# Optimization experiments

Measured on AMD Instinct MI355X. Metric: run time of the kernel, lower is better.

The kernel has to match this reference:

```python
import jax, jax.numpy as jnp
import numpy as np

INF = 1e9
GAMMA, ALPHA, RADIUS = 2.0, 0.25, 1.5
STRIDES = (8, 16, 32, 64, 128)
IMG = 256
SIZES = ((-1.0, 64.0), (64.0, 128.0), (128.0, 256.0), (256.0, 512.0), (512.0, INF))


def _level_meta():
    # per-level 3D point grids, stride*radius per point, size-of-interest per point
    pts, spt, soi = [], [], []
    for s, (lo, hi) in zip(STRIDES, SIZES):
        n = IMG // s
        ax = (np.arange(n) + 0.5) * s
        zz, yy, xx = np.meshgrid(ax, ax, ax, indexing='ij')
        p = np.stack([xx.ravel(), yy.ravel(), zz.ravel()], 1)
        pts.append(p)
        spt.append(np.full(p.shape[0], s * RADIUS))
        soi.append(np.tile(np.array([lo, hi]), (p.shape[0], 1)))
    return (np.concatenate(pts).astype(np.float32),
            np.concatenate(spt).astype(np.float32),
            np.concatenate(soi).astype(np.float32))


def setup_inputs() -> dict:
    key = jax.random.key(0)
    ks = jax.random.split(key, 8)
    B, G, C = 4, 48, 8
    loc_np, spt_np, soi_np = _level_meta()
    N = loc_np.shape[0]  # 37448
    ctr = jax.random.uniform(ks[0], (B, G, 3), minval=32.0, maxval=224.0)
    half = jax.random.uniform(ks[1], (B, G, 3), minval=8.0, maxval=96.0)
    bboxes = jnp.concatenate([ctr - half, ctr + half], -1)  # valid xyzxyz boxes
    return {
        'locations': jnp.asarray(loc_np),
        'cls_pred': jax.random.normal(ks[2], (B, N, C), dtype=jnp.float32),
        'box_pred': jax.random.uniform(ks[3], (B, N, 6), minval=1.0, maxval=64.0),
        'center_pred': jax.random.normal(ks[4], (B, N), dtype=jnp.float32),
        'bboxes': bboxes,
        'gt_labels': jax.random.randint(ks[5], (B, G), 1, C + 1, dtype=jnp.int32),
        'gt_centers': ctr,
        'strides_pt': jnp.asarray(spt_np),
        'soi': jnp.asarray(soi_np),
    }


def _targets_one_image(loc, spt, soi, bb, lab):
    # loc [N,3], bb [G,6] -> label [N], box_target [N,6]
    xs, ys, zs = loc[:, 0], loc[:, 1], loc[:, 2]
    l = xs[:, None] - bb[None, :, 0]
    t = ys[:, None] - bb[None, :, 1]
    f = zs[:, None] - bb[None, :, 2]
    r = bb[None, :, 3] - xs[:, None]
    b = bb[None, :, 4] - ys[:, None]
    a = bb[None, :, 5] - zs[:, None]
    box_t = jnp.stack([l, t, f, r, b, a], 2)  # [N,G,6]
    # center sampling (get_sample_region): clip center box by gt box, test inside
    c = (bb[:, :3] + bb[:, 3:]) * 0.5  # [G,3]
    s = spt[:, None, None]  # [N,1,1] stride*radius per location
    cmin = jnp.maximum(c[None] - s, bb[None, :, :3])  # [N,G,3]
    cmax = jnp.minimum(c[None] + s, bb[None, :, 3:])
    d = jnp.concatenate([loc[:, None] - cmin, cmax - loc[:, None]], -1)  # [N,G,6]
    is_in = d.min(-1) > 0
    max_t = box_t.max(2)
    cared = (max_t >= soi[:, :1]) & (max_t <= soi[:, 1:2])
    area = jnp.prod(bb[:, 3:] - bb[:, :3], -1)  # [G]
    l2a = jnp.where(is_in & cared, area[None], INF)
    gt_id = jnp.argmin(l2a, 1)
    min_a = jnp.min(l2a, 1)
    box_target = jnp.take_along_axis(box_t, gt_id[:, None, None], 1)[:, 0]
    label = jnp.where(min_a == INF, 0, lab[gt_id])
    return label, box_target


def _focal_sum(logits, labels):
    # SigmoidFocalLoss, class ids 1..C, label 0 = background
    C = logits.shape[1]
    cr = jnp.arange(1, C + 1)
    pos = labels[:, None] == cr[None, :]
    p = jax.nn.sigmoid(logits)
    lp = jax.nn.log_sigmoid(logits)
    lnp = jax.nn.log_sigmoid(-logits)
    loss = jnp.where(pos, -ALPHA * (1.0 - p) ** GAMMA * lp,
                     -(1.0 - ALPHA) * p ** GAMMA * lnp)
    return loss.sum()


def _centerness(bt):
    lr = bt[:, jnp.array([0, 3])]
    tb = bt[:, jnp.array([1, 4])]
    fb = bt[:, jnp.array([2, 5])]
    c = (lr.min(1) / lr.max(1)) * (tb.min(1) / tb.max(1)) * (fb.min(1) / fb.max(1))
    return jnp.sqrt(jnp.clip(c, 1e-8, 1.0))


def _iou_loss(pred, tgt):
    # 3D IoU loss on (l,t,f,r,b,a) distances, -log(iou)
    pv = (pred[:, 0] + pred[:, 3]) * (pred[:, 1] + pred[:, 4]) * (pred[:, 2] + pred[:, 5])
    tv = (tgt[:, 0] + tgt[:, 3]) * (tgt[:, 1] + tgt[:, 4]) * (tgt[:, 2] + tgt[:, 5])
    m = jnp.minimum(pred, tgt)
    inter = (m[:, 0] + m[:, 3]) * (m[:, 1] + m[:, 4]) * (m[:, 2] + m[:, 5])
    union = pv + tv - inter
    ious = (inter + 1.0) / (union + 1.0)
    return -jnp.log(jnp.maximum(ious, 1e-6))


def reference(locations, cls_pred, box_pred, center_pred, bboxes, gt_labels,
              gt_centers, strides_pt, soi):
    labels, box_targets = jax.vmap(
        lambda bb, lb: _targets_one_image(locations, strides_pt, soi, bb, lb)
    )(bboxes, gt_labels)
    B = cls_pred.shape[0]
    lf = labels.reshape(-1)
    cf = cls_pred.reshape(-1, cls_pred.shape[-1])
    bf = box_pred.reshape(-1, 6)
    btf = box_targets.reshape(-1, 6)
    ctf = center_pred.reshape(-1)
    pos = lf > 0
    num_pos = pos.sum()
    cls_loss = _focal_sum(cf, lf) / (num_pos + B).astype(jnp.float32)
    # sanitize negative targets at non-positive locations (they are masked out)
    bt_safe = jnp.where(pos[:, None], btf, 1.0)
    bp_safe = jnp.where(pos[:, None], bf, 1.0)
    ctr_t = _centerness(bt_safe)
    w = jnp.where(pos, ctr_t, 0.0)
    box_loss = (_iou_loss(bp_safe, bt_safe) * w).sum() / jnp.maximum(w.sum(), 1e-8)
    # BCEWithLogits on positives only
    bce = jnp.maximum(ctf, 0.0) - ctf * ctr_t + jnp.log1p(jnp.exp(-jnp.abs(ctf)))
    center_loss = (bce * pos).sum() / jnp.maximum(num_pos, 1).astype(jnp.float32)
    return jnp.stack([cls_loss, box_loss, center_loss])
```

## Files before the change

### kernel.cpp

```cpp
#include <hip/hip_runtime.h>
#include <math.h>

#define BLOCK 256
#define MAXG  64
#define NSUM  5

__device__ __forceinline__ void lvl_of(int i, int& lvl, int& base, int& k) {
    if (i < 32768)      { lvl = 0; base = 0;     k = 5; }
    else if (i < 36864) { lvl = 1; base = 32768; k = 4; }
    else if (i < 37376) { lvl = 2; base = 36864; k = 3; }
    else if (i < 37440) { lvl = 3; base = 37376; k = 2; }
    else                { lvl = 4; base = 37440; k = 1; }
}

__global__ __launch_bounds__(BLOCK) void fcos_main(
    const float* __restrict__ loc,
    const float* __restrict__ clsp,
    const float* __restrict__ boxp,
    const float* __restrict__ ctrp,
    const float* __restrict__ bboxes,
    const int*   __restrict__ glab,
    const float* __restrict__ spt,
    const float* __restrict__ soi,
    int N, int G, int C, int nblk,
    double* __restrict__ part)
{
    __shared__ float sbx[6][MAXG];
    __shared__ float sarea[MAXG];
    __shared__ unsigned int ssmap[MAXG];
    __shared__ unsigned long long smask[2][6][32];
    __shared__ float4 sP[2];
    __shared__ int sNb[2];
    __shared__ double sred[(BLOCK / 64) * NSUM];

    const int b    = blockIdx.y;
    const int blk0 = blockIdx.x * BLOCK;
    const int i    = blk0 + threadIdx.x;

    int lvlA, baseA, kA; lvl_of(blk0, lvlA, baseA, kA);
    int lvlB, baseB, kB; lvl_of(min(blk0 + BLOCK - 1, N - 1), lvlB, baseB, kB);
    const int nbank = (lvlB != lvlA) ? 2 : 1;

    float bx[6]; float areaT = 0.f; int labT = 0;
    if (threadIdx.x < G) {
        const float* p = bboxes + ((size_t)b * G + threadIdx.x) * 6;
        #pragma unroll
        for (int d = 0; d < 6; ++d) bx[d] = p[d];
        areaT = (bx[3] - bx[0]) * (bx[4] - bx[1]) * (bx[5] - bx[2]);
        sarea[threadIdx.x] = areaT;
        labT = glab[b * G + threadIdx.x];
    }
    if (threadIdx.x < 2) {
        const int bank = threadIdx.x;
        const int bs   = bank ? baseB : baseA;
        const int kk   = bank ? kB : kA;
        sP[bank]  = make_float4(spt[bs], soi[(size_t)bs * 2], soi[(size_t)bs * 2 + 1],
                                2.0f * loc[(size_t)bs * 3]);
        sNb[bank] = 1 << kk;
    }
    __syncthreads();

    if (threadIdx.x < G) {
        int rank = 0;
        for (int j = 0; j < G; ++j) {
            const float aj = sarea[j];
            rank += (aj < areaT) || (aj == areaT && j < (int)threadIdx.x);
        }
        #pragma unroll
        for (int d = 0; d < 6; ++d) sbx[d][rank] = bx[d];
        ssmap[rank] = ((unsigned)labT << 16) | (unsigned)threadIdx.x;
    }
    __syncthreads();

    for (int e = threadIdx.x; e < nbank * 192; e += BLOCK) {
        const int bank = e / 192;
        const int r_   = e % 192;
        const int a    = r_ >> 5;
        const int cell = r_ & 31;
        const int d    = (a >= 3) ? a - 3 : a;
        const float4 P = sP[bank];
        unsigned long long m = 0ull;
        if (cell < sNb[bank]) {
            const float v = (cell + 0.5f) * P.w;
            if (a < 3) {
                for (int g = 0; g < G; ++g) {
                    const float blo = sbx[d][g], bhi = sbx[d + 3][g];
                    const float c = (blo + bhi) * 0.5f;
                    const float L = fmaxf(fmaxf(c - P.x, blo), bhi - P.z);
                    const float H = fminf(fminf(c + P.x, bhi), blo + P.z);
                    m |= (unsigned long long)((v > L) & (v < H)) << g;
                }
            } else {
                for (int g = 0; g < G; ++g) {
                    const float blo = sbx[d][g], bhi = sbx[d + 3][g];
                    m |= (unsigned long long)((v > bhi - P.y) & (v < blo + P.y)) << g;
                }
            }
        }
        smask[bank][a][cell] = m;
    }
    __syncthreads();

    float cls = 0.f, box = 0.f, w = 0.f, ctr = 0.f, npv = 0.f;

    if (i < N) {
        int lvl, base, k; lvl_of(i, lvl, base, k);
        const int bank = (lvl == lvlA) ? 0 : 1;
        const int il  = i - base;
        const int nm1 = (1 << k) - 1;
        const int ix  = il & nm1;
        const int iy  = (il >> k) & nm1;
        const int iz  = il >> (2 * k);

        const unsigned long long el =
            (smask[bank][0][ix] & smask[bank][1][iy] & smask[bank][2][iz]) &
           ~(smask[bank][3][ix] & smask[bank][4][iy] & smask[bank][5][iz]);

        int label = 0, gidx = 0;
        if (el) {
            const int j = (int)__builtin_ctzll(el);
            const unsigned u = ssmap[j];
            label = (int)(u >> 16);
            gidx  = (int)(u & 0xffffu);
        }

        if (C == 8) {
            const float4 v0 = *(const float4*)(clsp + ((size_t)b * N + i) * 8);
            const float4 v1 = *(const float4*)(clsp + ((size_t)b * N + i) * 8 + 4);
            const float vv[8] = {v0.x, v0.y, v0.z, v0.w, v1.x, v1.y, v1.z, v1.w};
            #pragma unroll
            for (int c = 0; c < 8; ++c) {
                const float v = vv[c];
                const float e2  = __expf(-fabsf(v));
                const float sp  = __logf(1.0f + e2);
                const float lsm = fminf(v, 0.f) - sp;
                const float lsn = -fmaxf(v, 0.f) - sp;
                const float inv = 1.0f / (1.0f + e2);
                const float p   = (v >= 0.f) ? inv : e2 * inv;
                cls += (label == c + 1) ? -0.25f * (1.f - p) * (1.f - p) * lsm
                                        : -0.75f * p * p * lsn;
            }
        } else {
            for (int c = 0; c < C; ++c) {
                const float v = clsp[((size_t)b * N + i) * (size_t)C + c];
                const float e2  = __expf(-fabsf(v));
                const float sp  = __logf(1.0f + e2);
                const float lsm = fminf(v, 0.f) - sp;
                const float lsn = -fmaxf(v, 0.f) - sp;
                const float inv = 1.0f / (1.0f + e2);
                const float p   = (v >= 0.f) ? inv : e2 * inv;
                cls += (label == c + 1) ? -0.25f * (1.f - p) * (1.f - p) * lsm
                                        : -0.75f * p * p * lsn;
            }
        }

        if (label > 0) {
            const float x = loc[(size_t)i * 3 + 0];
            const float y = loc[(size_t)i * 3 + 1];
            const float z = loc[(size_t)i * 3 + 2];
            const float* pb = bboxes + ((size_t)b * G + gidx) * 6;
            const float b0 = pb[0], b1 = pb[1], b2 = pb[2];
            const float b3 = pb[3], b4 = pb[4], b5 = pb[5];
            const float l = x - b0, t  = y - b1, f = z - b2;
            const float r = b3 - x, bb = b4 - y, a = b5 - z;

            const float rx = fminf(l, r)  / fmaxf(l, r);
            const float ry = fminf(t, bb) / fmaxf(t, bb);
            const float rz = fminf(f, a)  / fmaxf(f, a);
            float c2 = rx * ry * rz;
            c2 = fminf(fmaxf(c2, 1e-8f), 1.0f);
            const float ct = sqrtf(c2);

            const float* bp = boxp + ((size_t)b * N + i) * 6;
            const float2 ba  = *(const float2*)(bp);
            const float2 bbv = *(const float2*)(bp + 2);
            const float2 bc  = *(const float2*)(bp + 4);
            const float p0 = ba.x,  p1 = ba.y,  p2 = bbv.x;
            const float p3 = bbv.y, p4 = bc.x,  p5 = bc.y;
            const float pv = (p0 + p3) * (p1 + p4) * (p2 + p5);
            const float tv = (l + r) * (t + bb) * (f + a);
            const float m0 = fminf(p0, l), m1 = fminf(p1, t),  m2 = fminf(p2, f);
            const float m3 = fminf(p3, r), m4 = fminf(p4, bb), m5 = fminf(p5, a);
            const float inter = (m0 + m3) * (m1 + m4) * (m2 + m5);
            const float uni2  = pv + tv - inter;
            const float iou   = (inter + 1.0f) / (uni2 + 1.0f);
            const float il2   = -__logf(fmaxf(iou, 1e-6f));
            box = il2 * ct;
            w   = ct;
            const float cv = ctrp[(size_t)b * N + i];
            ctr = fmaxf(cv, 0.f) - cv * ct + __logf(1.f + __expf(-fabsf(cv)));
            npv = 1.f;
        }
    }

    #pragma unroll
    for (int off = 32; off > 0; off >>= 1) {
        cls += __shfl_down(cls, off, 64);
        box += __shfl_down(box, off, 64);
        w   += __shfl_down(w,   off, 64);
        ctr += __shfl_down(ctr, off, 64);
        npv += __shfl_down(npv, off, 64);
    }
    const int wv = threadIdx.x >> 6;
    if ((threadIdx.x & 63) == 0) {
        sred[wv * NSUM + 0] = (double)cls;
        sred[wv * NSUM + 1] = (double)box;
        sred[wv * NSUM + 2] = (double)w;
        sred[wv * NSUM + 3] = (double)ctr;
        sred[wv * NSUM + 4] = (double)npv;
    }
    __syncthreads();
    if (threadIdx.x < NSUM) {
        double v = 0.0;
        #pragma unroll
        for (int k2 = 0; k2 < BLOCK / 64; ++k2) v += sred[k2 * NSUM + threadIdx.x];
        const int blk = blockIdx.y * gridDim.x + blockIdx.x;
        part[(size_t)threadIdx.x * nblk + blk] = v;
    }
}

__global__ __launch_bounds__(320) void fcos_final(
    const double* __restrict__ part, int nblk,
    float* __restrict__ out, int B)
{
    __shared__ double shm[NSUM];
    const int wv = threadIdx.x >> 6;
    const int ln = threadIdx.x & 63;
    double a = 0.0;
    const double* p = part + (size_t)wv * nblk;
    for (int k = ln; k < nblk; k += 64) a += p[k];
    #pragma unroll
    for (int off = 32; off > 0; off >>= 1) a += __shfl_down(a, off, 64);
    if (ln == 0) shm[wv] = a;
    __syncthreads();
    if (threadIdx.x == 0) {
        const double np = shm[4];
        out[0] = (float)(shm[0] / (np + (double)B));
        out[1] = (float)(shm[1] / fmax(shm[2], 1e-8));
        out[2] = (float)(shm[3] / fmax(np, 1.0));
    }
}

extern "C" void kernel_launch(void* const* d_in, const int* in_sizes, int n_in,
                              void* d_out, int out_size, void* d_ws, size_t ws_size,
                              hipStream_t stream) {
    const float* loc  = (const float*)d_in[0];
    const float* clsp = (const float*)d_in[1];
    const float* boxp = (const float*)d_in[2];
    const float* ctrp = (const float*)d_in[3];
    const float* bbox = (const float*)d_in[4];
    const int*   glab = (const int*)d_in[5];
    const float* spt  = (const float*)d_in[7];
    const float* soi  = (const float*)d_in[8];

    const int N = in_sizes[7];
    const int B = in_sizes[3] / N;
    const int G = in_sizes[5] / B;
    const int C = in_sizes[1] / in_sizes[3];

    const int gx   = (N + BLOCK - 1) / BLOCK;
    const int nblk = gx * B;
    double* part = (double*)d_ws;

    dim3 grid(gx, B);
    fcos_main<<<grid, BLOCK, 0, stream>>>(loc, clsp, boxp, ctrp, bbox, glab, spt, soi,
                                          N, G, C, nblk, part);
    fcos_final<<<1, 320, 0, stream>>>(part, nblk, (float*)d_out, B);
}
```

Baseline: 21.26 us.

## Fuse final reduction into main kernel via last-block atomic counter

Merges the two-kernel reduction into one kernel: each block writes partials, bumps a global counter, and the last block to arrive performs the final sum and writes the outputs. Block size grows from 256 to 1024, and the per-block sample-region masks are now precomputed for all five levels at once in a 62-cell table rather than per-bank. This removes a second kernel launch and its dependency gap, at the cost of heavier per-block mask setup, fewer blocks (lower parallelism), and reliance on a counter that is never reset, handled with a modulo.

```diff
diff --git a/kernel.cpp b/kernel.cpp
--- a/kernel.cpp
+++ b/kernel.cpp
@@ -1,9 +1,10 @@
 #include <hip/hip_runtime.h>
 #include <math.h>
 
-#define BLOCK 256
+#define BLOCK 1024
 #define MAXG  64
 #define NSUM  5
+#define NCELL 62
 
 __device__ __forceinline__ void lvl_of(int i, int& lvl, int& base, int& k) {
     if (i < 32768)      { lvl = 0; base = 0;     k = 5; }
@@ -12,8 +13,12 @@
     else if (i < 37440) { lvl = 3; base = 37376; k = 2; }
     else                { lvl = 4; base = 37440; k = 1; }
 }
-
-__global__ __launch_bounds__(BLOCK) void fcos_main(
+__device__ __forceinline__ int cell_base(int lvl) {
+    const int cb[5] = {0, 32, 48, 56, 60};
+    return cb[lvl];
+}
+
+__global__ __launch_bounds__(BLOCK) void fcos_fused(
     const float* __restrict__ loc,
     const float* __restrict__ clsp,
     const float* __restrict__ boxp,
@@ -22,24 +27,23 @@
     const int*   __restrict__ glab,
     const float* __restrict__ spt,
     const float* __restrict__ soi,
-    int N, int G, int C, int nblk,
-    double* __restrict__ part)
+    int N, int G, int C, int nblk, int B,
+    double* __restrict__ part,
+    unsigned int* __restrict__ cnt,
+    float* __restrict__ out)
 {
     __shared__ float sbx[6][MAXG];
     __shared__ float sarea[MAXG];
     __shared__ unsigned int ssmap[MAXG];
-    __shared__ unsigned long long smask[2][6][32];
-    __shared__ float4 sP[2];
-    __shared__ int sNb[2];
+    __shared__ unsigned long long smask[6][NCELL];
+    __shared__ float4 sP[5];
     __shared__ double sred[(BLOCK / 64) * NSUM];
-
-    const int b    = blockIdx.y;
-    const int blk0 = blockIdx.x * BLOCK;
-    const int i    = blk0 + threadIdx.x;
-
-    int lvlA, baseA, kA; lvl_of(blk0, lvlA, baseA, kA);
-    int lvlB, baseB, kB; lvl_of(min(blk0 + BLOCK - 1, N - 1), lvlB, baseB, kB);
-    const int nbank = (lvlB != lvlA) ? 2 : 1;
+    __shared__ double shm[NSUM];
+    __shared__ int sLast;
+
+    const int b   = blockIdx.y;
+    const int i   = blockIdx.x * BLOCK + threadIdx.x;
+    const int blk = blockIdx.y * gridDim.x + blockIdx.x;
 
     float bx[6]; float areaT = 0.f; int labT = 0;
     if (threadIdx.x < G) {
@@ -50,13 +54,11 @@
         sarea[threadIdx.x] = areaT;
         labT = glab[b * G + threadIdx.x];
     }
-    if (threadIdx.x < 2) {
-        const int bank = threadIdx.x;
-        const int bs   = bank ? baseB : baseA;
-        const int kk   = bank ? kB : kA;
-        sP[bank]  = make_float4(spt[bs], soi[(size_t)bs * 2], soi[(size_t)bs * 2 + 1],
-                                2.0f * loc[(size_t)bs * 3]);
-        sNb[bank] = 1 << kk;
+    if (threadIdx.x < 5) {
+        const int lb[5] = {0, 32768, 36864, 37376, 37440 - 8};
+        const int bs = lb[threadIdx.x];
+        sP[threadIdx.x] = make_float4(spt[bs], soi[(size_t)bs * 2],
+                                      soi[(size_t)bs * 2 + 1], 2.0f * loc[(size_t)bs * 3]);
     }
     __syncthreads();
 
@@ -72,32 +74,32 @@
     }
     __syncthreads();
 
-    for (int e = threadIdx.x; e < nbank * 192; e += BLOCK) {
-        const int bank = e / 192;
-        const int r_   = e % 192;
-        const int a    = r_ >> 5;
-        const int cell = r_ & 31;
-        const int d    = (a >= 3) ? a - 3 : a;
-        const float4 P = sP[bank];
+    if (threadIdx.x < 6 * NCELL) {
+        const int a  = threadIdx.x / NCELL;
+        const int gc = threadIdx.x % NCELL;
+        const int d  = (a >= 3) ? a - 3 : a;
+        int lvl;
+        if (gc < 32) lvl = 0; else if (gc < 48) lvl = 1;
+        else if (gc < 56) lvl = 2; else if (gc < 60) lvl = 3; else lvl = 4;
+        const int cell = gc - cell_base(lvl);
+        const float4 P = sP[lvl];
+        const float v = (cell + 0.5f) * P.w;
         unsigned long long m = 0ull;
-        if (cell < sNb[bank]) {
-            const float v = (cell + 0.5f) * P.w;
-            if (a < 3) {
-                for (int g = 0; g < G; ++g) {
-                    const float blo = sbx[d][g], bhi = sbx[d + 3][g];
-                    const float c = (blo + bhi) * 0.5f;
-                    const float L = fmaxf(fmaxf(c - P.x, blo), bhi - P.z);
-                    const float H = fminf(fminf(c + P.x, bhi), blo + P.z);
-                    m |= (unsigned long long)((v > L) & (v < H)) << g;
-                }
-            } else {
-                for (int g = 0; g < G; ++g) {
-                    const float blo = sbx[d][g], bhi = sbx[d + 3][g];
-                    m |= (unsigned long long)((v > bhi - P.y) & (v < blo + P.y)) << g;
-                }
-            }
-        }
-        smask[bank][a][cell] = m;
+        if (a < 3) {
+            for (int g = 0; g < G; ++g) {
+                const float blo = sbx[d][g], bhi = sbx[d + 3][g];
+                const float c = (blo + bhi) * 0.5f;
+                const float L = fmaxf(fmaxf(c - P.x, blo), bhi - P.z);
+                const float H = fminf(fminf(c + P.x, bhi), blo + P.z);
+                m |= (unsigned long long)((v > L) & (v < H)) << g;
+            }
+        } else {
+            for (int g = 0; g < G; ++g) {
+                const float blo = sbx[d][g], bhi = sbx[d + 3][g];
+                m |= (unsigned long long)((v > bhi - P.y) & (v < blo + P.y)) << g;
+            }
+        }
+        smask[a][gc] = m;
     }
     __syncthreads();
 
@@ -105,16 +107,16 @@
 
     if (i < N) {
         int lvl, base, k; lvl_of(i, lvl, base, k);
-        const int bank = (lvl == lvlA) ? 0 : 1;
+        const int cb  = cell_base(lvl);
         const int il  = i - base;
         const int nm1 = (1 << k) - 1;
-        const int ix  = il & nm1;
-        const int iy  = (il >> k) & nm1;
-        const int iz  = il >> (2 * k);
+        const int ix  = cb + (il & nm1);
+        const int iy  = cb + ((il >> k) & nm1);
+        const int iz  = cb + (il >> (2 * k));
 
         const unsigned long long el =
-            (smask[bank][0][ix] & smask[bank][1][iy] & smask[bank][2][iz]) &
-           ~(smask[bank][3][ix] & smask[bank][4][iy] & smask[bank][5][iz]);
+            (smask[0][ix] & smask[1][iy] & smask[2][iz]) &
+           ~(smask[3][ix] & smask[4][iy] & smask[5][iz]);
 
         int label = 0, gidx = 0;
         if (el) {
@@ -214,24 +216,29 @@
         double v = 0.0;
         #pragma unroll
         for (int k2 = 0; k2 < BLOCK / 64; ++k2) v += sred[k2 * NSUM + threadIdx.x];
-        const int blk = blockIdx.y * gridDim.x + blockIdx.x;
         part[(size_t)threadIdx.x * nblk + blk] = v;
     }
-}
-
-__global__ __launch_bounds__(320) void fcos_final(
-    const double* __restrict__ part, int nblk,
-    float* __restrict__ out, int B)
-{
-    __shared__ double shm[NSUM];
-    const int wv = threadIdx.x >> 6;
-    const int ln = threadIdx.x & 63;
-    double a = 0.0;
-    const double* p = part + (size_t)wv * nblk;
-    for (int k = ln; k < nblk; k += 64) a += p[k];
-    #pragma unroll
-    for (int off = 32; off > 0; off >>= 1) a += __shfl_down(a, off, 64);
-    if (ln == 0) shm[wv] = a;
+
+    if (threadIdx.x == 0) {
+        __threadfence();
+        const unsigned int old =
+            __hip_atomic_fetch_add(cnt, 1u, __ATOMIC_ACQ_REL, __HIP_MEMORY_SCOPE_AGENT);
+        sLast = (old % (unsigned int)nblk) == (unsigned int)(nblk - 1);
+    }
+    __syncthreads();
+    if (!sLast) return;
+
+    if (threadIdx.x < 64 * NSUM) {
+        const int j  = threadIdx.x >> 6;
+        const int ln = threadIdx.x & 63;
+        double a = 0.0;
+        for (int k2 = ln; k2 < nblk; k2 += 64)
+            a += __hip_atomic_load(&part[(size_t)j * nblk + k2],
+                                   __ATOMIC_RELAXED, __HIP_MEMORY_SCOPE_AGENT);
+        #pragma unroll
+        for (int off = 32; off > 0; off >>= 1) a += __shfl_down(a, off, 64);
+        if (ln == 0) shm[j] = a;
+    }
     __syncthreads();
     if (threadIdx.x == 0) {
         const double np = shm[4];
@@ -260,10 +267,11 @@
 
     const int gx   = (N + BLOCK - 1) / BLOCK;
     const int nblk = gx * B;
+
     double* part = (double*)d_ws;
+    unsigned int* cnt = (unsigned int*)((char*)d_ws + (size_t)NSUM * nblk * sizeof(double));
 
     dim3 grid(gx, B);
-    fcos_main<<<grid, BLOCK, 0, stream>>>(loc, clsp, boxp, ctrp, bbox, glab, spt, soi,
-                                          N, G, C, nblk, part);
-    fcos_final<<<1, 320, 0, stream>>>(part, nblk, (float*)d_out, B);
-}
+    fcos_fused<<<grid, BLOCK, 0, stream>>>(loc, clsp, boxp, ctrp, bbox, glab, spt, soi,
+                                           N, G, C, nblk, B, part, cnt, (float*)d_out);
+}
```

After: 20.60 us. -3.1%, faster.
